# Kernel tuning notes

Hardware: AMD Instinct MI355X
Metric: run time of the kernel (lower is better)

## Reference

```python
import jax, jax.numpy as jnp
import numpy as np
from jax import lax

DN = ('NHWC', 'HWIO', 'NHWC')

def conv2d_same(x, W, b):
    y = lax.conv_general_dilated(x, W, window_strides=(1, 1), padding='SAME', dimension_numbers=DN)
    return y + b

def maxpool2(x):
    # 2x2 max pool, stride 2, SAME padding (NHWC)
    return lax.reduce_window(x, -jnp.inf, lax.max, (1, 2, 2, 1), (1, 2, 2, 1), 'SAME')

def setup_inputs() -> dict:
    key = jax.random.key(0)
    ks = jax.random.split(key, 6)
    B, H, W, C = 8, 64, 64, 256
    s = 0.05
    return {
        'x': jax.random.normal(ks[0], (B, H, W, C), jnp.float32),
        'Wf': jax.random.normal(ks[1], (3, 3, C, C // 8), jnp.float32) * s,
        'bf': jnp.zeros((C // 8,), jnp.float32),
        'Wg': jax.random.normal(ks[2], (3, 3, C, C // 8), jnp.float32) * s,
        'bg': jnp.zeros((C // 8,), jnp.float32),
        'Wh': jax.random.normal(ks[3], (3, 3, C, C // 2), jnp.float32) * s,
        'bh': jnp.zeros((C // 2,), jnp.float32),
        'Wo': jax.random.normal(ks[4], (1, 1, C // 2, C), jnp.float32) * s,
        'bo': jnp.zeros((C,), jnp.float32),
        'gate': jnp.ones((1,), jnp.float32),
    }

def reference(x, Wf, bf, Wg, bg, Wh, bh, Wo, bo, gate):
    B, H, W, C = x.shape
    f = maxpool2(conv2d_same(x, Wf, bf))            # [B, H/2, W/2, C//8] keys
    g = conv2d_same(x, Wg, bg)                       # [B, H, W, C//8]     queries
    h = maxpool2(conv2d_same(x, Wh, bh))            # [B, H/2, W/2, C//2] values
    N, M = H * W, (H // 2) * (W // 2)
    gq = g.reshape(B, N, C // 8)
    fk = f.reshape(B, M, C // 8)
    hv = h.reshape(B, M, C // 2)
    attn = jax.nn.softmax(jnp.einsum('bnd,bmd->bnm', gq, fk), axis=-1)  # [B, N, M]
    wo = jnp.einsum('bnm,bmv->bnv', attn, hv).reshape(B, H, W, C // 2)
    out = conv2d_same(wo, Wo, bo)                    # [B, H, W, C]
    return x + gate[0] * out
```

## Files before the change

kernel.cpp:

```cpp
#include <hip/hip_runtime.h>
#include <hip/hip_fp16.h>

constexpr int B_  = 8;
constexpr int H_  = 64;
constexpr int W_  = 64;
constexpr int C_  = 256;
constexpr int CG_ = 32;
constexpr int CH_ = 128;
constexpr int NQ_ = 4096;
constexpr int NM_ = 1024;

constexpr int GP_ = 1048576;
constexpr int HP_ = 4194304;

typedef __attribute__((ext_vector_type(8))) _Float16 half8;
typedef __attribute__((ext_vector_type(4))) _Float16 half4;
typedef __attribute__((ext_vector_type(4))) float    f32x4;

__global__ void prep_w_k(const float* __restrict__ Wg, const float* __restrict__ Wf,
                         const float* __restrict__ Wh, const float* __restrict__ Wo,
                         const float* __restrict__ bg, const float* __restrict__ bf,
                         const float* __restrict__ bh,
                         _Float16* __restrict__ Wpk, _Float16* __restrict__ Wok,
                         float* __restrict__ bc) {
    int i = blockIdx.x * 256 + threadIdx.x;
    if (i < 12 * 9 * 8 * 64 * 8) {
        int j    = i & 7;
        int lane = (i >> 3) & 63;
        int ks   = (i >> 9) & 7;
        int tap  = (i >> 12) % 9;
        int co16 = i / 36864;
        int co = co16 * 16 + (lane & 15);
        int kk = tap * 256 + ks * 32 + (lane >> 4) * 8 + j;
        float v;
        if (co < 32)      v = Wg[(size_t)kk * 32  + co];
        else if (co < 64) v = Wf[(size_t)kk * 32  + (co - 32)];
        else              v = Wh[(size_t)kk * 128 + (co - 64)];
        Wpk[i] = (_Float16)v;
        return;
    }
    int i2 = i - 12 * 9 * 8 * 64 * 8;
    if (i2 < 16 * 4 * 64 * 8) {
        int j    = i2 & 7;
        int lane = (i2 >> 3) & 63;
        int ks   = (i2 >> 9) & 3;
        int co16 = i2 >> 11;
        int co = co16 * 16 + (lane & 15);
        int k  = ks * 32 + (lane >> 4) * 8 + j;
        Wok[i2] = (_Float16)Wo[(size_t)k * 256 + co];
        return;
    }
    int co = i2 - 16 * 4 * 64 * 8;
    if (co < 192)
        bc[co] = (co < 32) ? bg[co] : (co < 64) ? bf[co - 32] : bh[co - 64];
}

__global__ __launch_bounds__(512, 4) void conv_mfma_k(
        const float* __restrict__ X, const _Float16* __restrict__ Wpk,
        const float* __restrict__ bc,
        _Float16* __restrict__ gpart, _Float16* __restrict__ fpart,
        _Float16* __restrict__ hpart) {
    __shared__ char lds[2 * 32768];
    int bid = blockIdx.x;
    int lg  = (bid & 7) * 96 + (bid >> 3);
    int ky  = lg % 3;
    int ip  = lg / 3;
    int b   = ip >> 5;
    int y0  = (ip & 31) * 2;
    int tid = threadIdx.x;
    int wid = tid >> 6;
    int rid = wid >> 2;
    int nw  = wid & 3;
    int l   = tid & 63;
    int lr  = l & 15;
    int lk  = l >> 4;

    {
#pragma unroll
        for (int j = 0; j < 8; ++j) {
            int cc  = tid + j * 512;
            int row = cc >> 11;
            int c   = cc & 2047;
            int px  = c >> 5;
            int c8  = (c & 31) * 8;
            int yin = y0 + ky - 1 + row;
            half8 v = (half8)(_Float16)0.f;
            if (yin >= 0 && yin < 64) {
                const float* s = X + (((size_t)(b * 64 + yin) * 64) + px) * 256 + c8;
                float4 a  = *reinterpret_cast<const float4*>(s);
                float4 b2 = *reinterpret_cast<const float4*>(s + 4);
                v[0] = (_Float16)a.x;  v[1] = (_Float16)a.y;
                v[2] = (_Float16)a.z;  v[3] = (_Float16)a.w;
                v[4] = (_Float16)b2.x; v[5] = (_Float16)b2.y;
                v[6] = (_Float16)b2.z; v[7] = (_Float16)b2.w;
            }
            *reinterpret_cast<half8*>(lds + row * 32768 +
                ((c * 16) ^ ((px & 7) << 4))) = v;
        }
    }
    __syncthreads();

    f32x4 acc[4][3];
#pragma unroll
    for (int mi = 0; mi < 4; ++mi)
#pragma unroll
        for (int nj = 0; nj < 3; ++nj) acc[mi][nj] = (f32x4)0.f;

    int tap0 = ky * 3;
    const char* ldsr = lds + rid * 32768;

    auto ldw = [&](int s, half8* d) {
        const _Float16* p = Wpk +
            ((((size_t)(nw * 3) * 9 + tap0 + (s >> 3)) * 8 + (s & 7)) * 64 + l) * 8;
        d[0] = *reinterpret_cast<const half8*>(p);
        d[1] = *reinterpret_cast<const half8*>(p + 36864);
        d[2] = *reinterpret_cast<const half8*>(p + 73728);
    };

    half8 wb[2][3];
    ldw(0, wb[0]);
#pragma unroll
    for (int st = 0; st < 24; ++st) {
        if (st < 23) ldw(st + 1, wb[(st + 1) & 1]);
        int kx = st >> 3, ks = st & 7;
        half8 af[4];
#pragma unroll
        for (int mi = 0; mi < 4; ++mi) {
            int px  = mi * 16 + lr + kx - 1;
            int pxc = px < 0 ? 0 : (px > 63 ? 63 : px);
            int ad  = (pxc * 512 + ks * 64 + lk * 16) ^ ((pxc & 7) << 4);
            half8 a = *reinterpret_cast<const half8*>(ldsr + ad);
            if (px < 0 || px > 63) a = (half8)(_Float16)0.f;
            af[mi] = a;
        }
        const half8* w = wb[st & 1];
#pragma unroll
        for (int mi = 0; mi < 4; ++mi)
            acc[mi][0] = __builtin_amdgcn_mfma_f32_16x16x32_f16(af[mi], w[0], acc[mi][0], 0, 0, 0);
#pragma unroll
        for (int mi = 0; mi < 4; ++mi)
            acc[mi][1] = __builtin_amdgcn_mfma_f32_16x16x32_f16(af[mi], w[1], acc[mi][1], 0, 0, 0);
#pragma unroll
        for (int mi = 0; mi < 4; ++mi)
            acc[mi][2] = __builtin_amdgcn_mfma_f32_16x16x32_f16(af[mi], w[2], acc[mi][2], 0, 0, 0);
    }

    int pixbase = (b * 64 + y0 + rid) * 64;
    bool addb = (ky == 1);
#pragma unroll
    for (int nj = 0; nj < 3; ++nj) {
        int co = nw * 48 + nj * 16 + lr;
        float bias = addb ? bc[co] : 0.f;
#pragma unroll
        for (int mi = 0; mi < 4; ++mi) {
#pragma unroll
            for (int r = 0; r < 4; ++r) {
                int x = mi * 16 + lk * 4 + r;
                float v = acc[mi][nj][r] + bias;
                size_t pix = pixbase + x;
                if (co < 32)
                    gpart[(size_t)ky * GP_ + pix * 32 + co] = (_Float16)(v * 1.44269504f);
                else if (co < 64)
                    fpart[(size_t)ky * GP_ + pix * 32 + (co - 32)] = (_Float16)v;
                else
                    hpart[(size_t)ky * HP_ + pix * 128 + (co - 64)] = (_Float16)v;
            }
        }
    }
}

__global__ void maxpool_f16_k(const _Float16* __restrict__ fp, _Float16* __restrict__ dst) {
    int i = blockIdx.x * 256 + threadIdx.x;
    if (i >= B_ * NM_ * CG_) return;
    int c = i & 31;
    int t = i >> 5;
    int px = t & 31;
    int py = (t >> 5) & 31;
    int b  = t >> 10;
    size_t base = (((size_t)(b * 64 + py * 2)) * 64 + px * 2) * 32 + c;
    const _Float16* p1 = fp + GP_;
    const _Float16* p2 = fp + 2 * GP_;
    auto val = [&](size_t o) { return (float)fp[o] + (float)p1[o] + (float)p2[o]; };
    float v = fmaxf(fmaxf(val(base), val(base + 32)),
                    fmaxf(val(base + 64 * 32), val(base + 64 * 32 + 32)));
    dst[i] = (_Float16)v;
}

__global__ __launch_bounds__(256) void vtpool_k(const _Float16* __restrict__ hp,
                                                _Float16* __restrict__ Vt) {
    __shared__ float t[32][33];
    int b  = blockIdx.x >> 7;
    int kt = (blockIdx.x >> 2) & 31;
    int ct = blockIdx.x & 3;
    int tid = threadIdx.x;
    const _Float16* p1 = hp + HP_;
    const _Float16* p2 = hp + 2 * (size_t)HP_;
#pragma unroll
    for (int i = 0; i < 4; ++i) {
        int e = tid + i * 256;
        int px = e >> 5, c = e & 31;
        size_t base = (((size_t)(b * 64 + kt * 2) * 64) + px * 2) * 128 + ct * 32 + c;
        auto val = [&](size_t o) { return (float)hp[o] + (float)p1[o] + (float)p2[o]; };
        float v = fmaxf(fmaxf(val(base), val(base + 128)),
                        fmaxf(val(base + 64 * 128), val(base + 64 * 128 + 128)));
        t[px][c] = v;
    }
    __syncthreads();
#pragma unroll
    for (int i = 0; i < 4; ++i) {
        int e = tid + i * 256;
        int c = e >> 5, px = e & 31;
        Vt[((size_t)b * 128 + ct * 32 + c) * 1024 + kt * 32 + px] = (_Float16)t[px][c];
    }
}

constexpr int PP_ = 72;

__global__ __launch_bounds__(256, 2) void attn_flash_k(
        const _Float16* __restrict__ Qp,
        const _Float16* __restrict__ Kf,
        const _Float16* __restrict__ Vt,
        _Float16* __restrict__ wo) {
    __shared__ _Float16 plds[4][16][PP_];
    __shared__ _Float16 vlds[2][8192];
    int bb  = blockIdx.x >> 6;
    int qt  = blockIdx.x & 63;
    int wid = threadIdx.x >> 6;
    int l   = threadIdx.x & 63;
    int lr  = l & 15;
    int lg  = l >> 4;
    int qbase = qt * 64 + wid * 16;

    const _Float16* gp = Qp + ((size_t)bb * NQ_ + qbase + lr) * 32 + lg * 8;
    half8 bq = *reinterpret_cast<const half8*>(gp);
    bq = bq + *reinterpret_cast<const half8*>(gp + GP_);
    bq = bq + *reinterpret_cast<const half8*>(gp + 2 * GP_);

    const _Float16* Kb = Kf + (size_t)bb * NM_ * 32;
    const _Float16* Vb = Vt + (size_t)bb * 128 * NM_;

    int o0  = wid * 4096 + l * 16;
    int vr0 = o0 >> 7;
    int vc  = (o0 >> 4) & 7;
    int vsw = (vr0 & 7) << 4;
    int lsw = (lr & 7) << 4;

    f32x4 acc[8];
#pragma unroll
    for (int vt = 0; vt < 8; ++vt) acc[vt] = (f32x4)0.f;
    float m_run = -1.0e30f;
    float l_lane = 0.f;

    half8 ak0, ak1, ak2, ak3;
    f32x4 s0, s1, s2, s3;
    half4 ph0, ph1, ph2, ph3;
    float4 vst[4];

#define STAGE_LOAD(T)                                                              \
    {   const _Float16* vp = Vb + (size_t)(T) * 64 + (size_t)vr0 * NM_ + vc * 8;   \
        vst[0] = *reinterpret_cast<const float4*>(vp);                             \
        vst[1] = *reinterpret_cast<const float4*>(vp + 8 * NM_);                   \
        vst[2] = *reinterpret_cast<const float4*>(vp + 16 * NM_);                  \
        vst[3] = *reinterpret_cast<const float4*>(vp + 24 * NM_);                  \
    }

#define STAGE_WRITE(BUF)                                                           \
    {   char* vbp = (char*)vlds[BUF] + (o0 ^ vsw);                                 \
        *reinterpret_cast<float4*>(vbp)        = vst[0];                           \
        *reinterpret_cast<float4*>(vbp + 1024) = vst[1];                           \
        *reinterpret_cast<float4*>(vbp + 2048) = vst[2];                           \
        *reinterpret_cast<float4*>(vbp + 3072) = vst[3];                           \
    }

#define LOADK(T)                                                                   \
    {   const _Float16* kp = Kb + (size_t)(T) * 64 * 32;                           \
        ak0 = *reinterpret_cast<const half8*>(kp + (size_t)(lr)      * 32 + lg*8); \
        ak1 = *reinterpret_cast<const half8*>(kp + (size_t)(16 + lr) * 32 + lg*8); \
        ak2 = *reinterpret_cast<const half8*>(kp + (size_t)(32 + lr) * 32 + lg*8); \
        ak3 = *reinterpret_cast<const half8*>(kp + (size_t)(48 + lr) * 32 + lg*8); \
    }

#define QK()                                                                \
    {   s0 = __builtin_amdgcn_mfma_f32_16x16x32_f16(ak0, bq, (f32x4)0.f, 0, 0, 0); \
        s1 = __builtin_amdgcn_mfma_f32_16x16x32_f16(ak1, bq, (f32x4)0.f, 0, 0, 0); \
        s2 = __builtin_amdgcn_mfma_f32_16x16x32_f16(ak2, bq, (f32x4)0.f, 0, 0, 0); \
        s3 = __builtin_amdgcn_mfma_f32_16x16x32_f16(ak3, bq, (f32x4)0.f, 0, 0, 0); \
    }

#define SOFTMAX()                                                           \
    {   float lm = fmaxf(fmaxf(fmaxf(s0[0], s0[1]), fmaxf(s0[2], s0[3])),   \
                         fmaxf(fmaxf(s1[0], s1[1]), fmaxf(s1[2], s1[3])));  \
        lm = fmaxf(lm, fmaxf(fmaxf(fmaxf(s2[0], s2[1]), fmaxf(s2[2], s2[3])), \
                             fmaxf(fmaxf(s3[0], s3[1]), fmaxf(s3[2], s3[3])))); \
        if (__any(lm > m_run + 11.0f)) {                                    \
            float mx = lm;                                                  \
            mx = fmaxf(mx, __shfl_xor(mx, 16, 64));                         \
            mx = fmaxf(mx, __shfl_xor(mx, 32, 64));                         \
            float mnew  = fmaxf(m_run, mx);                                 \
            float alpha = exp2f(m_run - mnew);                              \
            l_lane *= alpha;                                                \
            _Pragma("unroll")                                               \
            for (int r = 0; r < 4; ++r) {                                   \
                float ar = __shfl(alpha, 4 * lg + r, 64);                   \
                _Pragma("unroll")                                           \
                for (int vt = 0; vt < 8; ++vt) acc[vt][r] *= ar;            \
            }                                                               \
            m_run = mnew;                                                   \
        }                                                                   \
        float ps = 0.f;                                                     \
        {   float p0 = exp2f(s0[0]-m_run), p1 = exp2f(s0[1]-m_run);         \
            float p2 = exp2f(s0[2]-m_run), p3 = exp2f(s0[3]-m_run);         \
            ps += (p0+p1)+(p2+p3);                                          \
            ph0[0]=(_Float16)p0; ph0[1]=(_Float16)p1;                       \
            ph0[2]=(_Float16)p2; ph0[3]=(_Float16)p3; }                     \
        {   float p0 = exp2f(s1[0]-m_run), p1 = exp2f(s1[1]-m_run);         \
            float p2 = exp2f(s1[2]-m_run), p3 = exp2f(s1[3]-m_run);         \
            ps += (p0+p1)+(p2+p3);                                          \
            ph1[0]=(_Float16)p0; ph1[1]=(_Float16)p1;                       \
            ph1[2]=(_Float16)p2; ph1[3]=(_Float16)p3; }                     \
        {   float p0 = exp2f(s2[0]-m_run), p1 = exp2f(s2[1]-m_run);         \
            float p2 = exp2f(s2[2]-m_run), p3 = exp2f(s2[3]-m_run);         \
            ps += (p0+p1)+(p2+p3);                                          \
            ph2[0]=(_Float16)p0; ph2[1]=(_Float16)p1;                       \
            ph2[2]=(_Float16)p2; ph2[3]=(_Float16)p3; }                     \
        {   float p0 = exp2f(s3[0]-m_run), p1 = exp2f(s3[1]-m_run);         \
            float p2 = exp2f(s3[2]-m_run), p3 = exp2f(s3[3]-m_run);         \
            ps += (p0+p1)+(p2+p3);                                          \
            ph3[0]=(_Float16)p0; ph3[1]=(_Float16)p1;                       \
            ph3[2]=(_Float16)p2; ph3[3]=(_Float16)p3; }                     \
        l_lane += ps;                                                       \
    }

#define WRITEP()                                                            \
    {   *reinterpret_cast<half4*>(&plds[wid][lr][ 0 + 4*lg]) = ph0;         \
        *reinterpret_cast<half4*>(&plds[wid][lr][16 + 4*lg]) = ph1;         \
        *reinterpret_cast<half4*>(&plds[wid][lr][32 + 4*lg]) = ph2;         \
        *reinterpret_cast<half4*>(&plds[wid][lr][48 + 4*lg]) = ph3;         \
    }

#define PV(BUF)                                                             \
    {   half8 ap0 = *reinterpret_cast<const half8*>(&plds[wid][lr][8*lg]);  \
        half8 ap1 = *reinterpret_cast<const half8*>(&plds[wid][lr][32 + 8*lg]); \
        const char* vbp = (const char*)vlds[BUF];                           \
        _Pragma("unroll")                                                   \
        for (int vt = 0; vt < 8; ++vt) {                                    \
            int ra = (vt * 16 + lr) * 128;                                  \
            half8 bv = *reinterpret_cast<const half8*>(                     \
                vbp + ((ra + lg * 16) ^ lsw));                              \
            acc[vt] = __builtin_amdgcn_mfma_f32_16x16x32_f16(ap0, bv, acc[vt], 0, 0, 0); \
        }                                                                   \
        _Pragma("unroll")                                                   \
        for (int vt = 0; vt < 8; ++vt) {                                    \
            int ra = (vt * 16 + lr) * 128;                                  \
            half8 bv = *reinterpret_cast<const half8*>(                     \
                vbp + ((ra + (4 + lg) * 16) ^ lsw));                        \
            acc[vt] = __builtin_amdgcn_mfma_f32_16x16x32_f16(ap1, bv, acc[vt], 0, 0, 0); \
        }                                                                   \
    }

    STAGE_LOAD(0);
    STAGE_WRITE(0);
    LOADK(0);
    __syncthreads();
    QK(); SOFTMAX();

    for (int t = 0; t < 16; ++t) {
        if (t < 15) { STAGE_LOAD(t + 1); LOADK(t + 1); }
        WRITEP();
        PV(t & 1);
        if (t < 15) STAGE_WRITE((t + 1) & 1);
        __syncthreads();
        if (t < 15) { QK(); SOFTMAX(); }
    }

#undef STAGE_LOAD
#undef STAGE_WRITE
#undef LOADK
#undef QK
#undef SOFTMAX
#undef WRITEP
#undef PV

    float lsum = l_lane;
    lsum += __shfl_xor(lsum, 16, 64);
    lsum += __shfl_xor(lsum, 32, 64);
    float inv = 1.f / lsum;
#pragma unroll
    for (int r = 0; r < 4; ++r) {
        float ir = __shfl(inv, 4 * lg + r, 64);
        _Float16* orow = wo + ((size_t)bb * NQ_ + qbase + 4 * lg + r) * 128 + lr;
#pragma unroll
        for (int vt = 0; vt < 8; ++vt) orow[vt * 16] = (_Float16)(acc[vt][r] * ir);
    }
}

__global__ __launch_bounds__(256, 2) void conv1x1_mfma_k(
        const _Float16* __restrict__ wo, const _Float16* __restrict__ Wok,
        const float* __restrict__ bo, const float* __restrict__ X,
        const float* __restrict__ gate, float* __restrict__ out) {
    __shared__ char lds[64 * 256];
    int pix0 = blockIdx.x * 64;
    int tid = threadIdx.x;
    int wq = tid >> 6;
    int l  = tid & 63;
    int lr = l & 15;
    int lg = l >> 4;

    {
        const float4* sp = reinterpret_cast<const float4*>(wo + (size_t)pix0 * 128);
#pragma unroll
        for (int j = 0; j < 4; ++j) {
            int c = tid + j * 256;
            int px = c >> 4;
            *reinterpret_cast<float4*>(lds + ((c * 16) ^ ((px & 7) << 4))) = sp[c];
        }
    }
    __syncthreads();

    f32x4 acc[4][4];
#pragma unroll
    for (int mi = 0; mi < 4; ++mi)
#pragma unroll
        for (int nj = 0; nj < 4; ++nj) acc[mi][nj] = (f32x4)0.f;

#pragma unroll
    for (int ks = 0; ks < 4; ++ks) {
        half8 ap[4];
#pragma unroll
        for (int mi = 0; mi < 4; ++mi) {
            int px = mi * 16 + lr;
            int ad = (px * 256 + ks * 64 + lg * 16) ^ ((px & 7) << 4);
            ap[mi] = *reinterpret_cast<const half8*>(lds + ad);
        }
#pragma unroll
        for (int nj = 0; nj < 4; ++nj) {
            int co16 = wq * 4 + nj;
            half8 bv = *reinterpret_cast<const half8*>(
                Wok + (((size_t)co16 * 4 + ks) * 64 + l) * 8);
#pragma unroll
            for (int mi = 0; mi < 4; ++mi)
                acc[mi][nj] = __builtin_amdgcn_mfma_f32_16x16x32_f16(ap[mi], bv, acc[mi][nj], 0, 0, 0);
        }
    }

    float gt = gate[0];
#pragma unroll
    for (int nj = 0; nj < 4; ++nj) {
        int co = wq * 64 + nj * 16 + lr;
        float bias = bo[co];
#pragma unroll
        for (int mi = 0; mi < 4; ++mi) {
#pragma unroll
            for (int r = 0; r < 4; ++r) {
                size_t o = (size_t)(pix0 + mi * 16 + lg * 4 + r) * 256 + co;
                out[o] = X[o] + gt * (acc[mi][nj][r] + bias);
            }
        }
    }
}

extern "C" void kernel_launch(void* const* d_in, const int* in_sizes, int n_in,
                              void* d_out, int out_size, void* d_ws, size_t ws_size,
                              hipStream_t stream) {
    const float* X    = (const float*)d_in[0];
    const float* Wf   = (const float*)d_in[1];
    const float* bf   = (const float*)d_in[2];
    const float* Wg   = (const float*)d_in[3];
    const float* bg   = (const float*)d_in[4];
    const float* Wh   = (const float*)d_in[5];
    const float* bh   = (const float*)d_in[6];
    const float* Wo   = (const float*)d_in[7];
    const float* bo   = (const float*)d_in[8];
    const float* gate = (const float*)d_in[9];
    float* out = (float*)d_out;

    _Float16* gpart = (_Float16*)d_ws;
    _Float16* fpart = gpart + 3 * (size_t)GP_;
    _Float16* hpart = fpart + 3 * (size_t)GP_;
    _Float16* Kf    = hpart + 3 * (size_t)HP_;
    _Float16* Vt    = Kf + 262144;
    _Float16* Wpk   = Vt + 1048576;
    float*    bc    = (float*)(Wpk + 442368);
    _Float16* Wok   = (_Float16*)(bc + 192);
    _Float16* wobuf = hpart;

    prep_w_k<<<(12*9*8*64*8 + 16*4*64*8 + 192 + 255) / 256, 256, 0, stream>>>(
        Wg, Wf, Wh, Wo, bg, bf, bh, Wpk, Wok, bc);
    conv_mfma_k<<<3 * B_ * 32, 512, 0, stream>>>(X, Wpk, bc, gpart, fpart, hpart);
    maxpool_f16_k<<<(B_ * NM_ * CG_ + 255) / 256, 256, 0, stream>>>(fpart, Kf);
    vtpool_k<<<B_ * 32 * 4, 256, 0, stream>>>(hpart, Vt);
    attn_flash_k<<<B_ * 64, 256, 0, stream>>>(gpart, Kf, Vt, wobuf);
    conv1x1_mfma_k<<<(B_ * NQ_) / 64, 256, 0, stream>>>(wobuf, Wok, bo, X, gate, out);
}
```

Baseline: 105.1 us.

## Prefetch conv A fragments, raise MFMA wave priority, merge pooling kernels

The 3x3 conv kernel now double-buffers its LDS A-fragment reads alongside the weight prefetch, so the next step's operands load while the current MFMAs run. MFMA blocks in the conv, QK and PV sections are wrapped in s_setprio(1)/s_setprio(0) to favour matrix-issuing waves. The two pooling kernels are merged into a single launch split by block index, which removes one launch. Holding the extra fragments raises register pressure, and the priority hints may have no effect or may disturb scheduling.

New measurement: 107.7 us. 1.02x slower.

```diff
diff --git a/kernel.cpp b/kernel.cpp
--- a/kernel.cpp
+++ b/kernel.cpp
@@ -116,14 +116,8 @@
         d[1] = *reinterpret_cast<const half8*>(p + 36864);
         d[2] = *reinterpret_cast<const half8*>(p + 73728);
     };
-
-    half8 wb[2][3];
-    ldw(0, wb[0]);
-#pragma unroll
-    for (int st = 0; st < 24; ++st) {
-        if (st < 23) ldw(st + 1, wb[(st + 1) & 1]);
-        int kx = st >> 3, ks = st & 7;
-        half8 af[4];
+    auto lda = [&](int s, half8* d) {
+        int kx = s >> 3, ks = s & 7;
 #pragma unroll
         for (int mi = 0; mi < 4; ++mi) {
             int px  = mi * 16 + lr + kx - 1;
@@ -131,9 +125,23 @@
             int ad  = (pxc * 512 + ks * 64 + lk * 16) ^ ((pxc & 7) << 4);
             half8 a = *reinterpret_cast<const half8*>(ldsr + ad);
             if (px < 0 || px > 63) a = (half8)(_Float16)0.f;
-            af[mi] = a;
-        }
-        const half8* w = wb[st & 1];
+            d[mi] = a;
+        }
+    };
+
+    half8 wb[2][3];
+    half8 afb[2][4];
+    ldw(0, wb[0]);
+    lda(0, afb[0]);
+#pragma unroll
+    for (int st = 0; st < 24; ++st) {
+        if (st < 23) {
+            ldw(st + 1, wb[(st + 1) & 1]);
+            lda(st + 1, afb[(st + 1) & 1]);
+        }
+        const half8* w  = wb[st & 1];
+        const half8* af = afb[st & 1];
+        __builtin_amdgcn_s_setprio(1);
 #pragma unroll
         for (int mi = 0; mi < 4; ++mi)
             acc[mi][0] = __builtin_amdgcn_mfma_f32_16x16x32_f16(af[mi], w[0], acc[mi][0], 0, 0, 0);
@@ -143,6 +151,7 @@
 #pragma unroll
         for (int mi = 0; mi < 4; ++mi)
             acc[mi][2] = __builtin_amdgcn_mfma_f32_16x16x32_f16(af[mi], w[2], acc[mi][2], 0, 0, 0);
+        __builtin_amdgcn_s_setprio(0);
     }
 
     int pixbase = (b * 64 + y0 + rid) * 64;
@@ -169,30 +178,33 @@
     }
 }
 
-__global__ void maxpool_f16_k(const _Float16* __restrict__ fp, _Float16* __restrict__ dst) {
-    int i = blockIdx.x * 256 + threadIdx.x;
-    if (i >= B_ * NM_ * CG_) return;
-    int c = i & 31;
-    int t = i >> 5;
-    int px = t & 31;
-    int py = (t >> 5) & 31;
-    int b  = t >> 10;
-    size_t base = (((size_t)(b * 64 + py * 2)) * 64 + px * 2) * 32 + c;
-    const _Float16* p1 = fp + GP_;
-    const _Float16* p2 = fp + 2 * GP_;
-    auto val = [&](size_t o) { return (float)fp[o] + (float)p1[o] + (float)p2[o]; };
-    float v = fmaxf(fmaxf(val(base), val(base + 32)),
-                    fmaxf(val(base + 64 * 32), val(base + 64 * 32 + 32)));
-    dst[i] = (_Float16)v;
-}
-
-__global__ __launch_bounds__(256) void vtpool_k(const _Float16* __restrict__ hp,
-                                                _Float16* __restrict__ Vt) {
+__global__ __launch_bounds__(256) void pools_k(const _Float16* __restrict__ fp,
+                                               const _Float16* __restrict__ hp,
+                                               _Float16* __restrict__ Kf,
+                                               _Float16* __restrict__ Vt) {
     __shared__ float t[32][33];
-    int b  = blockIdx.x >> 7;
-    int kt = (blockIdx.x >> 2) & 31;
-    int ct = blockIdx.x & 3;
+    int blk = blockIdx.x;
     int tid = threadIdx.x;
+    if (blk < 1024) {
+        int i = blk * 256 + tid;
+        int c = i & 31;
+        int t2 = i >> 5;
+        int px = t2 & 31;
+        int py = (t2 >> 5) & 31;
+        int b  = t2 >> 10;
+        size_t base = (((size_t)(b * 64 + py * 2)) * 64 + px * 2) * 32 + c;
+        const _Float16* p1 = fp + GP_;
+        const _Float16* p2 = fp + 2 * GP_;
+        auto val = [&](size_t o) { return (float)fp[o] + (float)p1[o] + (float)p2[o]; };
+        float v = fmaxf(fmaxf(val(base), val(base + 32)),
+                        fmaxf(val(base + 64 * 32), val(base + 64 * 32 + 32)));
+        Kf[i] = (_Float16)v;
+        return;
+    }
+    int bx = blk - 1024;
+    int b  = bx >> 7;
+    int kt = (bx >> 2) & 31;
+    int ct = bx & 3;
     const _Float16* p1 = hp + HP_;
     const _Float16* p2 = hp + 2 * (size_t)HP_;
 #pragma unroll
@@ -281,10 +293,12 @@
     }
 
 #define QK()                                                                \
-    {   s0 = __builtin_amdgcn_mfma_f32_16x16x32_f16(ak0, bq, (f32x4)0.f, 0, 0, 0); \
+    {   __builtin_amdgcn_s_setprio(1);                                      \
+        s0 = __builtin_amdgcn_mfma_f32_16x16x32_f16(ak0, bq, (f32x4)0.f, 0, 0, 0); \
         s1 = __builtin_amdgcn_mfma_f32_16x16x32_f16(ak1, bq, (f32x4)0.f, 0, 0, 0); \
         s2 = __builtin_amdgcn_mfma_f32_16x16x32_f16(ak2, bq, (f32x4)0.f, 0, 0, 0); \
         s3 = __builtin_amdgcn_mfma_f32_16x16x32_f16(ak3, bq, (f32x4)0.f, 0, 0, 0); \
+        __builtin_amdgcn_s_setprio(0);                                      \
     }
 
 #define SOFTMAX()                                                           \
@@ -342,6 +356,7 @@
     {   half8 ap0 = *reinterpret_cast<const half8*>(&plds[wid][lr][8*lg]);  \
         half8 ap1 = *reinterpret_cast<const half8*>(&plds[wid][lr][32 + 8*lg]); \
         const char* vbp = (const char*)vlds[BUF];                           \
+        __builtin_amdgcn_s_setprio(1);                                      \
         _Pragma("unroll")                                                   \
         for (int vt = 0; vt < 8; ++vt) {                                    \
             int ra = (vt * 16 + lr) * 128;                                  \
@@ -356,6 +371,7 @@
                 vbp + ((ra + (4 + lg) * 16) ^ lsw));                        \
             acc[vt] = __builtin_amdgcn_mfma_f32_16x16x32_f16(ap1, bv, acc[vt], 0, 0, 0); \
         }                                                                   \
+        __builtin_amdgcn_s_setprio(0);                                      \
     }
 
     STAGE_LOAD(0);
@@ -487,8 +503,7 @@
     prep_w_k<<<(12*9*8*64*8 + 16*4*64*8 + 192 + 255) / 256, 256, 0, stream>>>(
         Wg, Wf, Wh, Wo, bg, bf, bh, Wpk, Wok, bc);
     conv_mfma_k<<<3 * B_ * 32, 512, 0, stream>>>(X, Wpk, bc, gpart, fpart, hpart);
-    maxpool_f16_k<<<(B_ * NM_ * CG_ + 255) / 256, 256, 0, stream>>>(fpart, Kf);
-    vtpool_k<<<B_ * 32 * 4, 256, 0, stream>>>(hpart, Vt);
+    pools_k<<<2048, 256, 0, stream>>>(fpart, hpart, Kf, Vt);
     attn_flash_k<<<B_ * 64, 256, 0, stream>>>(gpart, Kf, Vt, wobuf);
     conv1x1_mfma_k<<<(B_ * NQ_) / 64, 256, 0, stream>>>(wobuf, Wok, bo, X, gate, out);
 }
```
